# Performance work log

Measured on AMD Instinct MI355X. Metric: run time of the kernel, lower is better.

## Reference

```python
import jax, jax.numpy as jnp
import numpy as np

HEAD_DIM = 64
N_HEADS = 16
D_S = N_HEADS * HEAD_DIM  # 1024
D_Z = 128


def setup_inputs() -> dict:
    key = jax.random.key(0)
    ks = jax.random.split(key, 12)
    B, S = 1, 1024
    sc = 0.02
    return {
        "s": jax.random.normal(ks[0], (B, S, D_S), jnp.float32),
        "z": jax.random.normal(ks[1], (B, S, S, D_Z), jnp.float32),
        "wq": jax.random.normal(ks[2], (N_HEADS * HEAD_DIM, D_S), jnp.float32) * sc,
        "bq": jax.random.normal(ks[3], (N_HEADS * HEAD_DIM,), jnp.float32) * sc,
        "wk": jax.random.normal(ks[4], (N_HEADS * HEAD_DIM, D_S), jnp.float32) * sc,
        "wv": jax.random.normal(ks[5], (N_HEADS * HEAD_DIM, D_S), jnp.float32) * sc,
        "wg": jax.random.normal(ks[6], (N_HEADS * HEAD_DIM, D_S), jnp.float32) * sc,
        "z_norm_w": jnp.ones((D_Z,), jnp.float32),
        "z_norm_b": jnp.zeros((D_Z,), jnp.float32),
        "wz": jax.random.normal(ks[7], (N_HEADS, D_Z), jnp.float32) * sc,
        "wo": jax.random.normal(ks[8], (D_S, N_HEADS * HEAD_DIM), jnp.float32) * sc,
    }


def _layer_norm(x, w, b, eps=1e-5):
    mu = jnp.mean(x, axis=-1, keepdims=True)
    var = jnp.var(x, axis=-1, keepdims=True)
    return (x - mu) * jax.lax.rsqrt(var + eps) * w + b


def reference(s, z, wq, bq, wk, wv, wg, z_norm_w, z_norm_b, wz, wo):
    B, S, _ = s.shape
    H, hd = N_HEADS, HEAD_DIM
    # fused QKV projection (only q has bias in the original)
    q = (s @ wq.T + bq).reshape(B, S, H, hd)
    k = (s @ wk.T).reshape(B, S, H, hd)
    v = (s @ wv.T).reshape(B, S, H, hd)
    # pair bias: LN(z) -> linear D_Z -> H, permute to [B,H,S,S]
    zn = _layer_norm(z, z_norm_w, z_norm_b)
    bias = jnp.einsum("bijz,hz->bhij", zn, wz)  # [B,H,S,S]
    # attention with pair bias (net math: qk/sqrt(d) + bias)
    scores = jnp.einsum("bihd,bjhd->bhij", q, k) * (hd ** -0.5) + bias
    attn = jax.nn.softmax(scores, axis=-1)
    o = jnp.einsum("bhij,bjhd->bihd", attn, v).reshape(B, S, H * hd)
    # sigmoid gate then output projection
    g = jax.nn.sigmoid(s @ wg.T)
    return (o * g) @ wo.T
```

## Files before the change

kernel.cpp:

```cpp
#include <hip/hip_runtime.h>

typedef __attribute__((ext_vector_type(8))) short bf16x8;
typedef __attribute__((ext_vector_type(4))) float f32x4;

#define MFMA16(a,b,c) __builtin_amdgcn_mfma_f32_16x16x32_bf16(a,b,c,0,0,0)

__device__ __forceinline__ unsigned short f2bf(float f){
  unsigned int u = __float_as_uint(f);
  unsigned int r = (u + 0x7fffu + ((u >> 16) & 1u)) >> 16;
  return (unsigned short)r;
}
__device__ __forceinline__ float bf2f(unsigned short u){
  return __uint_as_float(((unsigned int)u) << 16);
}

__global__ __launch_bounds__(256) void prep_kernel(
    const float* __restrict__ s, const float* __restrict__ wq,
    const float* __restrict__ wk, const float* __restrict__ wv,
    const float* __restrict__ wg, const float* __restrict__ wo,
    const float* __restrict__ wz, const float* __restrict__ znw,
    const float* __restrict__ znb,
    unsigned short* __restrict__ sb, unsigned short* __restrict__ Wp,
    unsigned short* __restrict__ wob,
    unsigned short* __restrict__ wzp, float* __restrict__ c12)
{
  __shared__ float r1[256], r2[256];
  if (blockIdx.x == 6144) {
    int t = threadIdx.x; int h = t >> 4; int k0 = (t & 15) * 8;
    float p1 = 0.f, p2 = 0.f;
    for (int e = 0; e < 8; e++) {
      float wvv = wz[h*128 + k0 + e];
      float w = znw[k0 + e], b = znb[k0 + e];
      wzp[h*128 + k0 + e] = f2bf(wvv * w);
      p1 += wvv * w; p2 += wvv * b;
    }
    r1[t] = p1; r2[t] = p2;
    __syncthreads();
    if ((t & 15) == 0) {
      float s1 = 0.f, s2 = 0.f;
      for (int i = 0; i < 16; i++) { s1 += r1[t + i]; s2 += r2[t + i]; }
      c12[2*h] = s1; c12[2*h + 1] = s2;
    }
    return;
  }
  const size_t M1 = 1u << 20;
  size_t base = ((size_t)blockIdx.x * 256 + threadIdx.x) * 4;
  const float* src; unsigned short* dst; size_t off;
  if (base < M1) { src = s; dst = sb; off = base; }
  else if (base < 5*M1) {
    size_t r = base - M1; int wsel = (int)(r >> 20);
    const float* wsrc0 = (wsel == 0) ? wq : (wsel == 1) ? wk : (wsel == 2) ? wv : wg;
    src = wsrc0; dst = Wp + ((size_t)wsel << 20); off = r & (M1 - 1);
  } else { src = wo; dst = wob; off = base - 5*M1; }
  float4 v = *(const float4*)(src + off);
  ushort4 o4;
  o4.x = f2bf(v.x); o4.y = f2bf(v.y); o4.z = f2bf(v.z); o4.w = f2bf(v.w);
  *(ushort4*)(dst + off) = o4;
}

template<int MODE>
__global__ __launch_bounds__(256) void gemm_bf16(
    const unsigned short* __restrict__ A, const unsigned short* __restrict__ Bm,
    int M, int N, int K,
    const float* __restrict__ bq,
    unsigned short* __restrict__ qb, unsigned short* __restrict__ kb,
    unsigned short* __restrict__ vT, unsigned short* __restrict__ gb,
    float* __restrict__ outF)
{
  int lane = threadIdx.x & 63;
  int w = threadIdx.x >> 6;
  int lr = lane & 15, lg = lane >> 4;
  int row0 = blockIdx.y * 64 + (w & 1) * 32;
  int col0 = blockIdx.x * 128 + (w >> 1) * 64;
  f32x4 acc[2][4] = {};
  for (int kk = 0; kk < K; kk += 32) {
    bf16x8 af[2], bfr[4];
    #pragma unroll
    for (int t = 0; t < 2; t++)
      af[t] = *(const bf16x8*)(A + (size_t)(row0 + t*16 + lr) * K + kk + lg*8);
    #pragma unroll
    for (int t = 0; t < 4; t++)
      bfr[t] = *(const bf16x8*)(Bm + (size_t)(col0 + t*16 + lr) * K + kk + lg*8);
    #pragma unroll
    for (int a = 0; a < 2; a++)
      #pragma unroll
      for (int b = 0; b < 4; b++)
        acc[a][b] = MFMA16(af[a], bfr[b], acc[a][b]);
  }
  #pragma unroll
  for (int a = 0; a < 2; a++)
    #pragma unroll
    for (int b = 0; b < 4; b++)
      #pragma unroll
      for (int r = 0; r < 4; r++) {
        int m = row0 + a*16 + lg*4 + r;
        int n = col0 + b*16 + lr;
        float v = acc[a][b][r];
        if (MODE == 0) {
          if (n < 1024)      { v = (v + bq[n]) * 0.125f; qb[(size_t)m*1024 + n] = f2bf(v); }
          else if (n < 2048) { kb[(size_t)m*1024 + (n-1024)] = f2bf(v); }
          else if (n < 3072) { vT[(size_t)(n-2048)*1024 + m] = f2bf(v); }
          else               { float sg = 1.f / (1.f + __expf(-v)); gb[(size_t)m*1024 + (n-3072)] = f2bf(sg); }
        } else {
          outF[(size_t)m * N + n] = v;
        }
      }
}

__global__ __launch_bounds__(1024, 4) void fused_attn(
    const unsigned short* __restrict__ qb, const unsigned short* __restrict__ kb,
    const unsigned short* __restrict__ vT, const float* __restrict__ z,
    const unsigned short* __restrict__ wzp, const float* __restrict__ c12,
    float* __restrict__ op, float* __restrict__ ml, float* __restrict__ ll)
{
  __shared__ float biasT[16][17][68];
  __shared__ unsigned short P[16][1024];
  int w = threadIdx.x >> 6;
  int lane = threadIdx.x & 63;
  int jl = lane & 15, g = lane >> 4;
  int q0 = blockIdx.x * 16;
  int s = blockIdx.y;
  int h = w;
  unsigned short* Pw = P[w];

  bf16x8 af[4];
  #pragma unroll
  for (int mk = 0; mk < 4; mk++)
    af[mk] = *(const bf16x8*)(wzp + jl*128 + mk*32 + g*8);
  bf16x8 aq[2];
  #pragma unroll
  for (int kh = 0; kh < 2; kh++)
    aq[kh] = *(const bf16x8*)(qb + (size_t)(q0 + jl)*1024 + h*64 + kh*32 + g*8);
  float c1r[4], c2r[4];
  #pragma unroll
  for (int r = 0; r < 4; r++) {
    c1r[r] = c12[2*(g*4 + r)];
    c2r[r] = c12[2*(g*4 + r) + 1];
  }

  f32x4 od[4] = {};
  float m = -1e30f, ss = 0.f;

  #pragma unroll 1
  for (int t = 0; t < 4; t++) {
    int jt = s*256 + t*64;

    #pragma unroll 1
    for (int it = 0; it < 4; it++) {
      int j = jt + it*16 + jl;
      const float* zp = z + ((size_t)(q0 + w)*1024 + j)*128;
      bf16x8 tf[4];
      float sum = 0.f, sq = 0.f;
      #pragma unroll
      for (int mk = 0; mk < 4; mk++) {
        float4 a = *(const float4*)(zp + mk*32 + g*8);
        float4 b = *(const float4*)(zp + mk*32 + g*8 + 4);
        sum += a.x + a.y + a.z + a.w + b.x + b.y + b.z + b.w;
        sq = fmaf(a.x, a.x, fmaf(a.y, a.y, fmaf(a.z, a.z, fmaf(a.w, a.w, sq))));
        sq = fmaf(b.x, b.x, fmaf(b.y, b.y, fmaf(b.z, b.z, fmaf(b.w, b.w, sq))));
        bf16x8 tv;
        tv[0] = (short)f2bf(a.x); tv[1] = (short)f2bf(a.y);
        tv[2] = (short)f2bf(a.z); tv[3] = (short)f2bf(a.w);
        tv[4] = (short)f2bf(b.x); tv[5] = (short)f2bf(b.y);
        tv[6] = (short)f2bf(b.z); tv[7] = (short)f2bf(b.w);
        tf[mk] = tv;
      }
      sum += __shfl_xor(sum, 16); sum += __shfl_xor(sum, 32);
      sq  += __shfl_xor(sq, 16);  sq  += __shfl_xor(sq, 32);
      float mu = sum * (1.f/128.f);
      float rs = rsqrtf(sq * (1.f/128.f) - mu*mu + 1e-5f);
      f32x4 D = {0.f, 0.f, 0.f, 0.f};
      #pragma unroll
      for (int mk = 0; mk < 4; mk++)
        D = MFMA16(af[mk], tf[mk], D);
      #pragma unroll
      for (int r = 0; r < 4; r++)
        biasT[g*4 + r][w][it*16 + jl] = rs*(D[r] - mu*c1r[r]) + c2r[r];
    }
    __syncthreads();

    f32x4 sc[4] = {};
    #pragma unroll
    for (int jb = 0; jb < 4; jb++)
      #pragma unroll
      for (int kh = 0; kh < 2; kh++) {
        bf16x8 bk = *(const bf16x8*)(kb + (size_t)(jt + jb*16 + jl)*1024 + h*64 + kh*32 + g*8);
        sc[jb] = MFMA16(bk, aq[kh], sc[jb]);
      }
    #pragma unroll
    for (int jb = 0; jb < 4; jb++) {
      f32x4 bl = *(const f32x4*)(&biasT[h][jl][jb*16 + g*4]);
      sc[jb][0] += bl[0]; sc[jb][1] += bl[1];
      sc[jb][2] += bl[2]; sc[jb][3] += bl[3];
    }

    float mx = -1e30f;
    #pragma unroll
    for (int jb = 0; jb < 4; jb++)
      #pragma unroll
      for (int r = 0; r < 4; r++) mx = fmaxf(mx, sc[jb][r]);
    mx = fmaxf(mx, __shfl_xor(mx, 16));
    mx = fmaxf(mx, __shfl_xor(mx, 32));
    float mn = fmaxf(m, mx);
    float a = __expf(m - mn);
    m = mn;
    float rsum = 0.f;
    #pragma unroll
    for (int jb = 0; jb < 4; jb++) {
      short4 pk;
      float p0 = __expf(sc[jb][0] - mn); rsum += p0; pk.x = (short)f2bf(p0);
      float p1 = __expf(sc[jb][1] - mn); rsum += p1; pk.y = (short)f2bf(p1);
      float p2 = __expf(sc[jb][2] - mn); rsum += p2; pk.z = (short)f2bf(p2);
      float p3 = __expf(sc[jb][3] - mn); rsum += p3; pk.w = (short)f2bf(p3);
      int b = jb*2 + (g >> 1);
      int bpz = b ^ (jl & 7);
      *(short4*)(Pw + jl*64 + bpz*8 + (g & 1)*4) = pk;
    }
    ss = ss * a + rsum;

    float albc[4];
    #pragma unroll
    for (int r = 0; r < 4; r++) albc[r] = __shfl(a, g*4 + r);
    #pragma unroll
    for (int db = 0; db < 4; db++)
      #pragma unroll
      for (int r = 0; r < 4; r++) od[db][r] *= albc[r];

    #pragma unroll
    for (int jh = 0; jh < 2; jh++) {
      int b = jh*4 + g;
      int bpz = b ^ (jl & 7);
      bf16x8 ap = *(const bf16x8*)(Pw + jl*64 + bpz*8);
      #pragma unroll
      for (int db = 0; db < 4; db++) {
        bf16x8 bv = *(const bf16x8*)(vT + (size_t)(h*64 + db*16 + jl)*1024 + jt + jh*32 + g*8);
        od[db] = MFMA16(ap, bv, od[db]);
      }
    }
    __syncthreads();
  }

  ss += __shfl_xor(ss, 16);
  ss += __shfl_xor(ss, 32);

  size_t base = ((size_t)(s*16 + h) * 1024);
  #pragma unroll
  for (int db = 0; db < 4; db++)
    #pragma unroll
    for (int r = 0; r < 4; r++) {
      int q = q0 + g*4 + r;
      op[(base + q)*64 + db*16 + jl] = od[db][r];
    }
  if (g == 0) {
    ml[base + q0 + jl] = m;
    ll[base + q0 + jl] = ss;
  }
}

__global__ __launch_bounds__(256) void combine_kernel(
    const float* __restrict__ op, const float* __restrict__ ml,
    const float* __restrict__ ll, const unsigned short* __restrict__ gb,
    unsigned short* __restrict__ og)
{
  int t = blockIdx.x * 256 + threadIdx.x;
  int d4 = t & 15;
  int q = (t >> 4) & 1023;
  int h = t >> 14;

  float mv[4], lv[4];
  float mstar = -1e30f;
  #pragma unroll
  for (int s = 0; s < 4; s++) {
    mv[s] = ml[(size_t)(s*16 + h)*1024 + q];
    lv[s] = ll[(size_t)(s*16 + h)*1024 + q];
    mstar = fmaxf(mstar, mv[s]);
  }
  float lsum = 0.f;
  float ws[4];
  #pragma unroll
  for (int s = 0; s < 4; s++) {
    ws[s] = __expf(mv[s] - mstar);
    lsum = fmaf(ws[s], lv[s], lsum);
  }
  float inv = 1.f / lsum;

  float4 o = {0.f, 0.f, 0.f, 0.f};
  #pragma unroll
  for (int s = 0; s < 4; s++) {
    float4 p = *(const float4*)(op + ((size_t)(s*16 + h)*1024 + q)*64 + d4*4);
    o.x = fmaf(ws[s], p.x, o.x); o.y = fmaf(ws[s], p.y, o.y);
    o.z = fmaf(ws[s], p.z, o.z); o.w = fmaf(ws[s], p.w, o.w);
  }
  ushort4 gv = *(const ushort4*)(gb + (size_t)q*1024 + h*64 + d4*4);
  ushort4 r;
  r.x = f2bf(o.x * inv * bf2f(gv.x));
  r.y = f2bf(o.y * inv * bf2f(gv.y));
  r.z = f2bf(o.z * inv * bf2f(gv.z));
  r.w = f2bf(o.w * inv * bf2f(gv.w));
  *(ushort4*)(og + (size_t)q*1024 + h*64 + d4*4) = r;
}

extern "C" void kernel_launch(void* const* d_in, const int* in_sizes, int n_in,
                              void* d_out, int out_size, void* d_ws, size_t ws_size,
                              hipStream_t stream) {
  const float* s   = (const float*)d_in[0];
  const float* z   = (const float*)d_in[1];
  const float* wq  = (const float*)d_in[2];
  const float* bq  = (const float*)d_in[3];
  const float* wk  = (const float*)d_in[4];
  const float* wv  = (const float*)d_in[5];
  const float* wg  = (const float*)d_in[6];
  const float* znw = (const float*)d_in[7];
  const float* znb = (const float*)d_in[8];
  const float* wz  = (const float*)d_in[9];
  const float* wo  = (const float*)d_in[10];
  float* out = (float*)d_out;

  char* ws = (char*)d_ws;
  unsigned short* qbuf  = (unsigned short*)(ws + ((size_t)64 << 20));
  unsigned short* kbuf  = (unsigned short*)(ws + ((size_t)66 << 20));
  unsigned short* vTb   = (unsigned short*)(ws + ((size_t)68 << 20));
  unsigned short* gbuf  = (unsigned short*)(ws + ((size_t)70 << 20));
  unsigned short* ogb   = (unsigned short*)(ws + ((size_t)72 << 20));
  unsigned short* sb    = (unsigned short*)(ws + ((size_t)74 << 20));
  unsigned short* Wp    = (unsigned short*)(ws + ((size_t)76 << 20));
  unsigned short* wob   = (unsigned short*)(ws + ((size_t)84 << 20));
  unsigned short* wzp   = (unsigned short*)(ws + ((size_t)86 << 20));
  float*          c12   = (float*)(ws + ((size_t)86 << 20) + 4096);
  float*          opart = (float*)(ws + ((size_t)96 << 20));
  float*          mlb   = (float*)(ws + ((size_t)112 << 20));
  float*          llb   = (float*)(ws + ((size_t)113 << 20));

  prep_kernel<<<6145, 256, 0, stream>>>(s, wq, wk, wv, wg, wo, wz, znw, znb,
                                        sb, Wp, wob, wzp, c12);
  gemm_bf16<0><<<dim3(32, 16), 256, 0, stream>>>(sb, Wp, 1024, 4096, 1024, bq,
                                                 qbuf, kbuf, vTb, gbuf, nullptr);
  fused_attn<<<dim3(64, 4), 1024, 0, stream>>>(qbuf, kbuf, vTb, z, wzp, c12,
                                               opart, mlb, llb);
  combine_kernel<<<1024, 256, 0, stream>>>(opart, mlb, llb, gbuf, ogb);
  gemm_bf16<1><<<dim3(8, 16), 256, 0, stream>>>(ogb, wob, 1024, 1024, 1024, nullptr,
                                                nullptr, nullptr, nullptr, nullptr, out);
}
```

Baseline: 229.1 us.

## Split pair-bias computation into streaming kernel with async LDS double-buffering

Moves the LayerNorm-plus-projection of z out of the fused attention kernel into a separate bias_stream kernel. That kernel streams z through double-buffered LDS using global_load_lds with a swizzled layout and writes a bf16 bias tensor [H,S,S] to workspace. The attention kernel becomes a lighter 256-thread kernel that reads the precomputed bias from global memory, with no block-wide syncs and more blocks. The goal is to hide the 512MB z read behind async prefetch, at the cost of an extra 32MB bias write and read round-trip and bf16 rounding of the bias.

```diff
diff --git a/kernel.cpp b/kernel.cpp
--- a/kernel.cpp
+++ b/kernel.cpp
@@ -12,6 +12,14 @@
 }
 __device__ __forceinline__ float bf2f(unsigned short u){
   return __uint_as_float(((unsigned int)u) << 16);
+}
+__device__ __forceinline__ bf16x8 cvt8(float4 a, float4 b){
+  bf16x8 t;
+  t[0] = (short)f2bf(a.x); t[1] = (short)f2bf(a.y);
+  t[2] = (short)f2bf(a.z); t[3] = (short)f2bf(a.w);
+  t[4] = (short)f2bf(b.x); t[5] = (short)f2bf(b.y);
+  t[6] = (short)f2bf(b.z); t[7] = (short)f2bf(b.w);
+  return t;
 }
 
 __global__ __launch_bounds__(256) void prep_kernel(
@@ -58,6 +66,98 @@
   *(ushort4*)(dst + off) = o4;
 }
 
+__global__ __launch_bounds__(512) void bias_stream(
+    const float* __restrict__ z, const unsigned short* __restrict__ wzp,
+    const float* __restrict__ c12, unsigned short* __restrict__ bias)
+{
+  __shared__ __align__(1024) char zbuf[2 * 65536];
+  __shared__ __align__(16) unsigned short bounce[8][16][20];
+  int tid = threadIdx.x;
+  int w = tid >> 6, lane = tid & 63;
+  int jl = lane & 15, g = lane >> 4;
+  int half = lane >> 5, lane31 = lane & 31;
+
+  bf16x8 af[4];
+  #pragma unroll
+  for (int mk = 0; mk < 4; mk++)
+    af[mk] = *(const bf16x8*)(wzp + jl*128 + mk*32 + g*8);
+  float c1r[4], c2r[4];
+  #pragma unroll
+  for (int r = 0; r < 4; r++) {
+    c1r[r] = c12[2*(g*4 + r)];
+    c2r[r] = c12[2*(g*4 + r) + 1];
+  }
+  int hp = lane & 15, gp = lane >> 4;
+
+  const int nsteps = 32;
+  int W = blockIdx.x * 8 + w;
+  int u0 = W * nsteps;
+
+  auto stage = [&](int u, int buf) {
+    int i = u >> 6, j16 = u & 63;
+    const char* gw = (const char*)z + (((size_t)i*1024 + j16*16) << 9);
+    char* lb = zbuf + buf*65536 + w*8192;
+    #pragma unroll
+    for (int c = 0; c < 8; c++) {
+      int row = c*2 + half;
+      unsigned pin = (unsigned)(lane31*16) ^ (unsigned)((row & 7) << 4);
+      __builtin_amdgcn_global_load_lds(
+          (const unsigned int*)(gw + (size_t)row*512 + pin),
+          (unsigned int*)(lb + c*1024), 16, 0, 0);
+    }
+  };
+
+  stage(u0, 0);
+  #pragma unroll 1
+  for (int step = 0; step < nsteps; ++step) {
+    int u = u0 + step;
+    int buf = step & 1;
+    if (step + 1 < nsteps) {
+      stage(u + 1, buf ^ 1);
+      asm volatile("s_waitcnt vmcnt(8)" ::: "memory");
+    } else {
+      asm volatile("s_waitcnt vmcnt(1)" ::: "memory");
+    }
+    __builtin_amdgcn_sched_barrier(0);
+
+    const char* wb = zbuf + buf*65536 + w*8192;
+    unsigned key = (unsigned)((jl & 7) << 4);
+    float sum = 0.f, sq = 0.f;
+    bf16x8 tf[4];
+    #pragma unroll
+    for (int mk = 0; mk < 4; mk++) {
+      unsigned x = (unsigned)(mk*128 + g*32);
+      float4 a = *(const float4*)(wb + jl*512 + (x ^ key));
+      float4 b = *(const float4*)(wb + jl*512 + ((x + 16) ^ key));
+      sum += a.x + a.y + a.z + a.w + b.x + b.y + b.z + b.w;
+      sq = fmaf(a.x, a.x, fmaf(a.y, a.y, fmaf(a.z, a.z, fmaf(a.w, a.w, sq))));
+      sq = fmaf(b.x, b.x, fmaf(b.y, b.y, fmaf(b.z, b.z, fmaf(b.w, b.w, sq))));
+      tf[mk] = cvt8(a, b);
+    }
+    sum += __shfl_xor(sum, 16); sum += __shfl_xor(sum, 32);
+    sq  += __shfl_xor(sq, 16);  sq  += __shfl_xor(sq, 32);
+    float mu = sum * (1.f/128.f);
+    float rs = rsqrtf(sq * (1.f/128.f) - mu*mu + 1e-5f);
+    f32x4 D = {0.f, 0.f, 0.f, 0.f};
+    #pragma unroll
+    for (int mk = 0; mk < 4; mk++)
+      D = MFMA16(af[mk], tf[mk], D);
+
+    #pragma unroll
+    for (int r = 0; r < 4; r++)
+      bounce[w][g*4 + r][jl] = f2bf(rs*(D[r] - mu*c1r[r]) + c2r[r]);
+    asm volatile("s_waitcnt lgkmcnt(0)" ::: "memory");
+    __builtin_amdgcn_sched_barrier(0);
+    {
+      int i = u >> 6, j16 = u & 63;
+      ushort4 vv = *(const ushort4*)(&bounce[w][hp][gp*4]);
+      *(ushort4*)(bias + ((size_t)hp << 20) + (size_t)i*1024 + j16*16 + gp*4) = vv;
+    }
+    asm volatile("s_waitcnt lgkmcnt(0)" ::: "memory");
+    __builtin_amdgcn_sched_barrier(0);
+  }
+}
+
 template<int MODE>
 __global__ __launch_bounds__(256) void gemm_bf16(
     const unsigned short* __restrict__ A, const unsigned short* __restrict__ Bm,
@@ -107,78 +207,29 @@
       }
 }
 
-__global__ __launch_bounds__(1024, 4) void fused_attn(
+__global__ __launch_bounds__(256) void attn_kernel(
     const unsigned short* __restrict__ qb, const unsigned short* __restrict__ kb,
-    const unsigned short* __restrict__ vT, const float* __restrict__ z,
-    const unsigned short* __restrict__ wzp, const float* __restrict__ c12,
+    const unsigned short* __restrict__ vT, const unsigned short* __restrict__ bias,
     float* __restrict__ op, float* __restrict__ ml, float* __restrict__ ll)
 {
-  __shared__ float biasT[16][17][68];
-  __shared__ unsigned short P[16][1024];
-  int w = threadIdx.x >> 6;
+  __shared__ unsigned short P[4][1024];
   int lane = threadIdx.x & 63;
+  int s = threadIdx.x >> 6;
   int jl = lane & 15, g = lane >> 4;
   int q0 = blockIdx.x * 16;
-  int s = blockIdx.y;
-  int h = w;
-  unsigned short* Pw = P[w];
-
-  bf16x8 af[4];
-  #pragma unroll
-  for (int mk = 0; mk < 4; mk++)
-    af[mk] = *(const bf16x8*)(wzp + jl*128 + mk*32 + g*8);
+  int h = blockIdx.y;
+  unsigned short* Pw = P[s];
+
   bf16x8 aq[2];
   #pragma unroll
   for (int kh = 0; kh < 2; kh++)
     aq[kh] = *(const bf16x8*)(qb + (size_t)(q0 + jl)*1024 + h*64 + kh*32 + g*8);
-  float c1r[4], c2r[4];
-  #pragma unroll
-  for (int r = 0; r < 4; r++) {
-    c1r[r] = c12[2*(g*4 + r)];
-    c2r[r] = c12[2*(g*4 + r) + 1];
-  }
 
   f32x4 od[4] = {};
   float m = -1e30f, ss = 0.f;
-
-  #pragma unroll 1
-  for (int t = 0; t < 4; t++) {
-    int jt = s*256 + t*64;
-
-    #pragma unroll 1
-    for (int it = 0; it < 4; it++) {
-      int j = jt + it*16 + jl;
-      const float* zp = z + ((size_t)(q0 + w)*1024 + j)*128;
-      bf16x8 tf[4];
-      float sum = 0.f, sq = 0.f;
-      #pragma unroll
-      for (int mk = 0; mk < 4; mk++) {
-        float4 a = *(const float4*)(zp + mk*32 + g*8);
-        float4 b = *(const float4*)(zp + mk*32 + g*8 + 4);
-        sum += a.x + a.y + a.z + a.w + b.x + b.y + b.z + b.w;
-        sq = fmaf(a.x, a.x, fmaf(a.y, a.y, fmaf(a.z, a.z, fmaf(a.w, a.w, sq))));
-        sq = fmaf(b.x, b.x, fmaf(b.y, b.y, fmaf(b.z, b.z, fmaf(b.w, b.w, sq))));
-        bf16x8 tv;
-        tv[0] = (short)f2bf(a.x); tv[1] = (short)f2bf(a.y);
-        tv[2] = (short)f2bf(a.z); tv[3] = (short)f2bf(a.w);
-        tv[4] = (short)f2bf(b.x); tv[5] = (short)f2bf(b.y);
-        tv[6] = (short)f2bf(b.z); tv[7] = (short)f2bf(b.w);
-        tf[mk] = tv;
-      }
-      sum += __shfl_xor(sum, 16); sum += __shfl_xor(sum, 32);
-      sq  += __shfl_xor(sq, 16);  sq  += __shfl_xor(sq, 32);
-      float mu = sum * (1.f/128.f);
-      float rs = rsqrtf(sq * (1.f/128.f) - mu*mu + 1e-5f);
-      f32x4 D = {0.f, 0.f, 0.f, 0.f};
-      #pragma unroll
-      for (int mk = 0; mk < 4; mk++)
-        D = MFMA16(af[mk], tf[mk], D);
-      #pragma unroll
-      for (int r = 0; r < 4; r++)
-        biasT[g*4 + r][w][it*16 + jl] = rs*(D[r] - mu*c1r[r]) + c2r[r];
-    }
-    __syncthreads();
-
+  const unsigned short* bp = bias + ((size_t)h << 20);
+
+  for (int jt = s*256; jt < s*256 + 256; jt += 64) {
     f32x4 sc[4] = {};
     #pragma unroll
     for (int jb = 0; jb < 4; jb++)
@@ -189,9 +240,9 @@
       }
     #pragma unroll
     for (int jb = 0; jb < 4; jb++) {
-      f32x4 bl = *(const f32x4*)(&biasT[h][jl][jb*16 + g*4]);
-      sc[jb][0] += bl[0]; sc[jb][1] += bl[1];
-      sc[jb][2] += bl[2]; sc[jb][3] += bl[3];
+      ushort4 bl = *(const ushort4*)(bp + (size_t)(q0 + jl)*1024 + jt + jb*16 + g*4);
+      sc[jb][0] += bf2f(bl.x); sc[jb][1] += bf2f(bl.y);
+      sc[jb][2] += bf2f(bl.z); sc[jb][3] += bf2f(bl.w);
     }
 
     float mx = -1e30f;
@@ -237,7 +288,6 @@
         od[db] = MFMA16(ap, bv, od[db]);
       }
     }
-    __syncthreads();
   }
 
   ss += __shfl_xor(ss, 16);
@@ -317,6 +367,7 @@
   float* out = (float*)d_out;
 
   char* ws = (char*)d_ws;
+  unsigned short* biasb = (unsigned short*)ws;
   unsigned short* qbuf  = (unsigned short*)(ws + ((size_t)64 << 20));
   unsigned short* kbuf  = (unsigned short*)(ws + ((size_t)66 << 20));
   unsigned short* vTb   = (unsigned short*)(ws + ((size_t)68 << 20));
@@ -335,8 +386,8 @@
                                         sb, Wp, wob, wzp, c12);
   gemm_bf16<0><<<dim3(32, 16), 256, 0, stream>>>(sb, Wp, 1024, 4096, 1024, bq,
                                                  qbuf, kbuf, vTb, gbuf, nullptr);
-  fused_attn<<<dim3(64, 4), 1024, 0, stream>>>(qbuf, kbuf, vTb, z, wzp, c12,
-                                               opart, mlb, llb);
+  bias_stream<<<256, 512, 0, stream>>>(z, wzp, c12, biasb);
+  attn_kernel<<<dim3(64, 16), 256, 0, stream>>>(qbuf, kbuf, vTb, biasb, opart, mlb, llb);
   combine_kernel<<<1024, 256, 0, stream>>>(opart, mlb, llb, gbuf, ogb);
   gemm_bf16<1><<<dim3(8, 16), 256, 0, stream>>>(ogb, wob, 1024, 1024, 1024, nullptr,
                                                 nullptr, nullptr, nullptr, nullptr, out);
```

After: 269.5 us. 17.6% more time.
